# Performance work log

Hardware: AMD Instinct MI355X
Metric: run time of the kernel (lower is better)

The kernel has to match this reference:

```python
import jax, jax.numpy as jnp
import numpy as np


def _normalize(x, axis=-1, eps=1e-12):
    n = jnp.linalg.norm(x, axis=axis, keepdims=True)
    return x / jnp.maximum(n, eps)


def _mlp(x, w1, b1, w2, b2):
    return jnp.maximum(x @ w1 + b1, 0.0) @ w2 + b2


def _quat_mul(a, b):
    # openfold (w, x, y, z) convention, Hamilton product
    aw, ax, ay, az = a[..., 0], a[..., 1], a[..., 2], a[..., 3]
    bw, bx, by, bz = b[..., 0], b[..., 1], b[..., 2], b[..., 3]
    return jnp.stack([
        aw * bw - ax * bx - ay * by - az * bz,
        aw * bx + ax * bw + ay * bz - az * by,
        aw * by - ax * bz + ay * bw + az * bx,
        aw * bz + ax * by - ay * bx + az * bw], axis=-1)


def _quat_rotate(q, v):
    # rotate vector v by unit quaternion q
    w = q[..., :1]
    u = q[..., 1:]
    t = 2.0 * jnp.cross(u, v)
    return v + w * t + jnp.cross(u, t)


def _conj(q):
    return q * jnp.asarray([1.0, -1.0, -1.0, -1.0], dtype=q.dtype)


def setup_inputs() -> dict:
    B, N, P, H, E, M = 2, 384, 128, 64, 32, 64
    key = jax.random.key(0)
    ks = iter(jax.random.split(key, 64))

    def nrm(shape):
        return jax.random.normal(next(ks), shape, dtype=jnp.float32)

    inp = {
        "frames_q": _normalize(nrm((B, N, 4))),
        "frames_x": nrm((B, N, 3)),
        "torsions": nrm((B, N, 7, 2)),
        "h": nrm((B, N, H)),
        "e": nrm((B, N, N, E)),
        "node_mask": jnp.ones((B, N), dtype=bool),
        "pocket_h": nrm((B, P, H)),
        "pocket_e": nrm((B, N, P, E)),
        "pocket_q": _normalize(nrm((B, P, 4))),
        "pocket_x": nrm((B, P, 3)),
        "pocket_mask": jnp.ones((B, P), dtype=bool),
    }
    # 2-layer MLPs with transition_size = 64
    for name, (fin, fout) in {"msg": (2 * H + E + 9, M), "feat": (H + M, H),
                              "tr": (M, 3), "qu": (M, 4), "to": (M, 14)}.items():
        inp[f"{name}_w1"] = nrm((fin, 64)) / np.sqrt(fin)
        inp[f"{name}_b1"] = nrm((64,)) * 0.01
        inp[f"{name}_w2"] = nrm((64, fout)) / np.sqrt(64)
        inp[f"{name}_b2"] = nrm((fout,)) * 0.01
    return inp


def reference(frames_q, frames_x, torsions, h, e, node_mask, pocket_h, pocket_e,
              pocket_q, pocket_x, pocket_mask,
              msg_w1, msg_b1, msg_w2, msg_b2,
              feat_w1, feat_b1, feat_w2, feat_b2,
              tr_w1, tr_b1, tr_w2, tr_b2,
              qu_w1, qu_b1, qu_w2, qu_b2,
              to_w1, to_b1, to_w2, to_b2):
    B, N, Hd = h.shape
    P = pocket_h.shape[-2]

    q_all = jnp.concatenate([frames_q, pocket_q], axis=-2)  # [B, N+P, 4]
    x_all = jnp.concatenate([frames_x, pocket_x], axis=-2)  # [B, N+P, 3]

    eye = jnp.eye(N, dtype=bool)
    mm = jnp.concatenate([
        node_mask[:, :, None] & node_mask[:, None, :] & ~eye,
        node_mask[:, :, None] & pocket_mask[:, None, :]], axis=-1)  # [B, N, N+P]

    vec = frames_x[:, :, None, :] - x_all[:, None, :, :]  # [B, N, N+P, 3]
    d2 = jnp.sum(vec * vec, axis=-1)                       # [B, N, N+P]
    qdot = jnp.abs(jnp.sum(frames_q[:, :, None, :] * q_all[:, None, :, :], axis=-1))

    # global -> local frame of node j applied to node i: R_j^T (x_i - t_j)
    qc = _conj(q_all)[:, None, :, :]                       # [B, 1, N+P, 4]
    local_x = _quat_rotate(qc, vec)                        # [B, N, N+P, 3]
    local_q = _quat_mul(qc, jnp.broadcast_to(frames_q[:, :, None, :], (B, N, N + P, 4)))

    feat = jnp.concatenate([
        jnp.broadcast_to(h[:, :, None, :], (B, N, N + P, Hd)),
        jnp.broadcast_to(jnp.concatenate([h, pocket_h], axis=-2)[:, None, :, :], (B, N, N + P, Hd)),
        jnp.concatenate([e, pocket_e], axis=-2),
        local_x, local_q, d2[..., None], qdot[..., None]], axis=-1)

    m = _mlp(feat, msg_w1, msg_b1, msg_w2, msg_b2) * mm[..., None]  # [B, N, N+P, M]
    msum = jnp.sum(m, axis=-2)                                      # [B, N, M]

    o = _mlp(jnp.concatenate([h, msum], axis=-1), feat_w1, feat_b1, feat_w2, feat_b2)

    dx = _mlp(m, tr_w1, tr_b1, tr_w2, tr_b2) * mm[..., None]        # [B, N, N+P, 3]

    ident = jnp.asarray([1.0, 0.0, 0.0, 0.0], dtype=frames_q.dtype)
    dq = _mlp(msum, qu_w1, qu_b1, qu_w2, qu_b2)
    dq = _normalize(jnp.where(node_mask[..., None], dq, ident))
    upd_q = _quat_mul(frames_q, dq)
    upd_q = _normalize(jnp.where(node_mask[..., None], upd_q, ident))

    qn_all = _normalize(q_all)
    gdx = jnp.sum(_quat_rotate(qn_all[:, None, :, :], dx), axis=-2)  # [B, N, 3]
    n_nb = (node_mask.sum(-1) + pocket_mask.sum(-1) - 1).astype(frames_x.dtype)
    upd_x = frames_x + gdx / n_nb[:, None, None]

    upd_torsions = _normalize(_mlp(msum, to_w1, to_b1, to_w2, to_b2).reshape(torsions.shape))

    return upd_q, upd_x, upd_torsions, o
```

## Files before the change

kernel.cpp:

```cpp
#include <hip/hip_runtime.h>
#include <math.h>

#define BB 2
#define NN 384
#define PP 128
#define HH 64
#define EE 32
#define NP 512
#define K1S 136
#define K2S 72

#define X_OFF (BB*NN*4)
#define T_OFF (X_OFF + BB*NN*3)
#define O_OFF (T_OFF + BB*NN*14)

using bf16x8 = __attribute__((ext_vector_type(8))) __bf16;
using f32x4  = __attribute__((ext_vector_type(4))) float;

__device__ __forceinline__ f32x4 MFMA(bf16x8 a, bf16x8 b, f32x4 c) {
  return __builtin_amdgcn_mfma_f32_16x16x32_bf16(a, b, c, 0, 0, 0);
}
__device__ __forceinline__ bf16x8 LDF(const __bf16* base, int off) {
  return *(const bf16x8*)(base + off);
}
__device__ __forceinline__ bf16x8 pack8(f32x4 lo, f32x4 hi) {
  bf16x8 r;
  r[0]=(__bf16)lo[0]; r[1]=(__bf16)lo[1]; r[2]=(__bf16)lo[2]; r[3]=(__bf16)lo[3];
  r[4]=(__bf16)hi[0]; r[5]=(__bf16)hi[1]; r[6]=(__bf16)hi[2]; r[7]=(__bf16)hi[3];
  return r;
}
__device__ __forceinline__ bf16x8 pack8v(float4 lo, float4 hi) {
  bf16x8 r;
  r[0]=(__bf16)lo.x; r[1]=(__bf16)lo.y; r[2]=(__bf16)lo.z; r[3]=(__bf16)lo.w;
  r[4]=(__bf16)hi.x; r[5]=(__bf16)hi.y; r[6]=(__bf16)hi.z; r[7]=(__bf16)hi.w;
  return r;
}
__device__ __forceinline__ int rowpos(int n) {
  const int t = (n>>5)*2 + ((n>>2)&1);
  const int q = ((n>>3)&3)*4 + (n&3);
  return t*16 + q;
}

__global__ __launch_bounds__(512, 2) void egnn_edge_swapped(
    const float* __restrict__ frames_q, const float* __restrict__ frames_x,
    const float* __restrict__ h, const float* __restrict__ e,
    const int* __restrict__ node_mask,
    const float* __restrict__ pocket_h, const float* __restrict__ pe,
    const float* __restrict__ pocket_q, const float* __restrict__ pocket_x,
    const int* __restrict__ pocket_mask,
    const float* __restrict__ w1, const float* __restrict__ b1,
    const float* __restrict__ w2, const float* __restrict__ b2,
    const float* __restrict__ tw1, const float* __restrict__ tb1,
    const float* __restrict__ tw2, const float* __restrict__ tb2,
    float* __restrict__ msum_ws, float* __restrict__ gdx_ws)
{
  __shared__ __align__(16) __bf16 s_w1p[64*K1S];
  __shared__ __align__(16) __bf16 s_w2p[64*K2S];
  __shared__ __align__(16) __bf16 s_tw1p[64*K2S];
  __shared__ __align__(16) __bf16 s_tw2p[16*K2S];
  __shared__ __align__(16) __bf16 s_geo[NP*16 + 8];
  __shared__ __align__(16) float s_qn[NP*4];
  __shared__ float s_maskf[NP];
  __shared__ __align__(16) float s_b2[64], s_tb1[64];
  __shared__ float s_tb2[4];
  __shared__ float s_msum[64], s_gdx[3];

  const int tid = threadIdx.x;
  const int b = blockIdx.x / NN, i = blockIdx.x % NN;

  for (int idx = tid; idx < 64*128; idx += 512) {
    const int n = idx & 63, k = idx >> 6;
    float v = 0.f;
    if      (k < 64)  v = w1[(64 + k)*64 + n];
    else if (k < 96)  v = w1[(128 + (k-64))*64 + n];
    else if (k < 105) v = w1[(160 + (k-96))*64 + n];
    if (k != 105) s_w1p[rowpos(n)*K1S + k] = (__bf16)v;
  }
  for (int idx = tid; idx < 64*64; idx += 512) {
    const int n = idx & 63, k = idx >> 6;
    s_w2p[rowpos(n)*K2S + k]  = (__bf16)w2[k*64 + n];
    s_tw1p[rowpos(n)*K2S + k] = (__bf16)tw1[k*64 + n];
  }
  for (int idx = tid; idx < 16*64; idx += 512) {
    const int row = idx >> 6, k = idx & 63;
    s_tw2p[row*K2S + k] = (__bf16)((row < 3) ? tw2[k*3 + row] : 0.f);
  }
  if (tid < 64) { s_b2[tid] = b2[tid]; s_tb1[tid] = tb1[tid]; s_msum[tid] = 0.f; }
  if (tid < 8)  s_geo[NP*16 + tid] = (__bf16)0.f;
  if (tid < 3)  { s_tb2[tid] = tb2[tid]; s_gdx[tid] = 0.f; }

  {
    const int n = tid >> 3, part = tid & 7;
    const float* hi = &h[(b*NN + i)*HH];
    float a = 0.f;
#pragma unroll
    for (int c = 0; c < 8; ++c) a = fmaf(hi[part*8 + c], w1[(part*8 + c)*64 + n], a);
    a += __shfl_xor(a, 1); a += __shfl_xor(a, 2); a += __shfl_xor(a, 4);
    if (part == 0) s_w1p[rowpos(n)*K1S + 105] = (__bf16)(a + b1[n]);
  }

  {
    const int j = tid;
    const int maski = node_mask[b*NN + i];
    const float qi0 = frames_q[(b*NN+i)*4+0], qi1 = frames_q[(b*NN+i)*4+1],
                qi2 = frames_q[(b*NN+i)*4+2], qi3 = frames_q[(b*NN+i)*4+3];
    const float xi0 = frames_x[(b*NN+i)*3+0], xi1 = frames_x[(b*NN+i)*3+1],
                xi2 = frames_x[(b*NN+i)*3+2];
    float qj0,qj1,qj2,qj3, xj0,xj1,xj2; int mj;
    if (j < NN) {
      const float4 q4 = *(const float4*)&frames_q[(b*NN+j)*4];
      qj0=q4.x; qj1=q4.y; qj2=q4.z; qj3=q4.w;
      xj0=frames_x[(b*NN+j)*3+0]; xj1=frames_x[(b*NN+j)*3+1]; xj2=frames_x[(b*NN+j)*3+2];
      mj = (node_mask[b*NN+j] != 0) && (j != i);
    } else {
      const int jp = j - NN;
      const float4 q4 = *(const float4*)&pocket_q[(b*PP+jp)*4];
      qj0=q4.x; qj1=q4.y; qj2=q4.z; qj3=q4.w;
      xj0=pocket_x[(b*PP+jp)*3+0]; xj1=pocket_x[(b*PP+jp)*3+1]; xj2=pocket_x[(b*PP+jp)*3+2];
      mj = (pocket_mask[b*PP+jp] != 0);
    }
    const float v0 = xi0 - xj0, v1 = xi1 - xj1, v2 = xi2 - xj2;
    const float d2 = v0*v0 + v1*v1 + v2*v2;
    const float qdot = fabsf(qi0*qj0 + qi1*qj1 + qi2*qj2 + qi3*qj3);
    const float cw = qj0, cx = -qj1, cy = -qj2, cz = -qj3;
    const float t0 = 2.f*(cy*v2 - cz*v1);
    const float t1 = 2.f*(cz*v0 - cx*v2);
    const float t2 = 2.f*(cx*v1 - cy*v0);
    const float lx0 = v0 + cw*t0 + (cy*t2 - cz*t1);
    const float lx1 = v1 + cw*t1 + (cz*t0 - cx*t2);
    const float lx2 = v2 + cw*t2 + (cx*t1 - cy*t0);
    const float lq0 = cw*qi0 - cx*qi1 - cy*qi2 - cz*qi3;
    const float lq1 = cw*qi1 + cx*qi0 + cy*qi3 - cz*qi2;
    const float lq2 = cw*qi2 - cx*qi3 + cy*qi0 + cz*qi1;
    const float lq3 = cw*qi3 + cx*qi2 - cy*qi1 + cz*qi0;
    __bf16* g = &s_geo[j*16];
    g[0]=(__bf16)lx0; g[1]=(__bf16)lx1; g[2]=(__bf16)lx2; g[3]=(__bf16)lq0;
    g[4]=(__bf16)lq1; g[5]=(__bf16)lq2; g[6]=(__bf16)lq3; g[7]=(__bf16)d2;
    g[8]=(__bf16)qdot; g[9]=(__bf16)1.f;
    g[10]=(__bf16)0.f; g[11]=(__bf16)0.f; g[12]=(__bf16)0.f;
    g[13]=(__bf16)0.f; g[14]=(__bf16)0.f; g[15]=(__bf16)0.f;
    s_maskf[j] = (maski && mj) ? 1.f : 0.f;
    const float inv = 1.f / fmaxf(sqrtf(qj0*qj0 + qj1*qj1 + qj2*qj2 + qj3*qj3), 1e-12f);
    float4* qn = (float4*)&s_qn[j*4];
    *qn = make_float4(qj0*inv, qj1*inv, qj2*inv, qj3*inv);
  }
  __syncthreads();

  const int wv = tid >> 6, lane = tid & 63;
  const int l15 = lane & 15, lg = lane >> 4;

  bf16x8 tw2f[2];
  tw2f[0] = *(const bf16x8*)&s_tw2p[l15*K2S +  0 + lg*8];
  tw2f[1] = *(const bf16x8*)&s_tw2p[l15*K2S + 32 + lg*8];
  const float tb2r0 = s_tb2[0], tb2r1 = s_tb2[1], tb2r2 = s_tb2[2];

  float msacc[16];
#pragma unroll
  for (int v = 0; v < 16; ++v) msacc[v] = 0.f;
  float gx0 = 0.f, gx1 = 0.f, gx2 = 0.f;

  const int o1base = l15*K1S + lg*8;
  const int o2base = l15*K2S + lg*8;
  const int obbase = lg*8;

#define LOADSTRIP(JB0, H0_,H1_,H2_,H3_,E0_,E1_) do {                        \
    const int jb_ = (JB0);                                                  \
    const int j_ = jb_ + l15;                                               \
    const float *hj_, *ej_;                                                 \
    if (jb_ < NN) {                                                         \
      hj_ = &h[(b*NN + j_)*HH];                                             \
      ej_ = &e[((b*NN + i)*NN + j_)*EE];                                    \
    } else {                                                                \
      const int jp_ = j_ - NN;                                              \
      hj_ = &pocket_h[(b*PP + jp_)*HH];                                     \
      ej_ = &pe[((b*NN + i)*PP + jp_)*EE];                                  \
    }                                                                       \
    H0_ = *(const float4*)&hj_[lg*8];                                       \
    H1_ = *(const float4*)&hj_[lg*8 + 4];                                   \
    H2_ = *(const float4*)&hj_[32 + lg*8];                                  \
    H3_ = *(const float4*)&hj_[32 + lg*8 + 4];                              \
    E0_ = *(const float4*)&ej_[lg*8];                                       \
    E1_ = *(const float4*)&ej_[lg*8 + 4];                                   \
  } while (0)

#pragma unroll
  for (int ss = 0; ss < 2; ++ss) {
    int o1 = o1base; asm volatile("" : "+v"(o1));
    int o2 = o2base; asm volatile("" : "+v"(o2));
    int ob = obbase; asm volatile("" : "+v"(ob));

    const int jbA = wv*64 + ss*32;
    const int jbB = jbA + 16;
    const int jA = jbA + l15, jB = jbB + l15;

    float4 hA0,hA1,hA2,hA3,eA0,eA1, hB0,hB1,hB2,hB3,eB0,eB1;
    LOADSTRIP(jbA, hA0,hA1,hA2,hA3,eA0,eA1);
    LOADSTRIP(jbB, hB0,hB1,hB2,hB3,eB0,eB1);
    const float maskA = s_maskf[jA];
    const float maskB = s_maskf[jB];

    const bf16x8 bfA0 = pack8v(hA0, hA1);
    const bf16x8 bfA1 = pack8v(hA2, hA3);
    const bf16x8 bfA2 = pack8v(eA0, eA1);
    const bf16x8 bfA3 = *(const bf16x8*)&s_geo[(lg < 2) ? (jA*16 + lg*8) : NP*16];
    const bf16x8 bfB0 = pack8v(hB0, hB1);
    const bf16x8 bfB1 = pack8v(hB2, hB3);
    const bf16x8 bfB2 = pack8v(eB0, eB1);
    const bf16x8 bfB3 = *(const bf16x8*)&s_geo[(lg < 2) ? (jB*16 + lg*8) : NP*16];

    const f32x4 zero4 = {0.f, 0.f, 0.f, 0.f};

    bf16x8 hbA0, hbA1, hbB0, hbB1;
    {
      f32x4 aA0, aA1, aB0, aB1;
      {
        const bf16x8 F0 = LDF(s_w1p, o1 + 0*16*K1S +  0);
        const bf16x8 F1 = LDF(s_w1p, o1 + 0*16*K1S + 32);
        const bf16x8 F2 = LDF(s_w1p, o1 + 0*16*K1S + 64);
        const bf16x8 F3 = LDF(s_w1p, o1 + 0*16*K1S + 96);
        aA0 = MFMA(F0,bfA0,zero4); aA0 = MFMA(F1,bfA1,aA0); aA0 = MFMA(F2,bfA2,aA0); aA0 = MFMA(F3,bfA3,aA0);
        aB0 = MFMA(F0,bfB0,zero4); aB0 = MFMA(F1,bfB1,aB0); aB0 = MFMA(F2,bfB2,aB0); aB0 = MFMA(F3,bfB3,aB0);
      }
      {
        const bf16x8 F0 = LDF(s_w1p, o1 + 1*16*K1S +  0);
        const bf16x8 F1 = LDF(s_w1p, o1 + 1*16*K1S + 32);
        const bf16x8 F2 = LDF(s_w1p, o1 + 1*16*K1S + 64);
        const bf16x8 F3 = LDF(s_w1p, o1 + 1*16*K1S + 96);
        aA1 = MFMA(F0,bfA0,zero4); aA1 = MFMA(F1,bfA1,aA1); aA1 = MFMA(F2,bfA2,aA1); aA1 = MFMA(F3,bfA3,aA1);
        aB1 = MFMA(F0,bfB0,zero4); aB1 = MFMA(F1,bfB1,aB1); aB1 = MFMA(F2,bfB2,aB1); aB1 = MFMA(F3,bfB3,aB1);
      }
#pragma unroll
      for (int r = 0; r < 4; ++r) {
        aA0[r] = fmaxf(aA0[r], 0.f); aA1[r] = fmaxf(aA1[r], 0.f);
        aB0[r] = fmaxf(aB0[r], 0.f); aB1[r] = fmaxf(aB1[r], 0.f);
      }
      hbA0 = pack8(aA0, aA1); hbB0 = pack8(aB0, aB1);
      {
        const bf16x8 F0 = LDF(s_w1p, o1 + 2*16*K1S +  0);
        const bf16x8 F1 = LDF(s_w1p, o1 + 2*16*K1S + 32);
        const bf16x8 F2 = LDF(s_w1p, o1 + 2*16*K1S + 64);
        const bf16x8 F3 = LDF(s_w1p, o1 + 2*16*K1S + 96);
        aA0 = MFMA(F0,bfA0,zero4); aA0 = MFMA(F1,bfA1,aA0); aA0 = MFMA(F2,bfA2,aA0); aA0 = MFMA(F3,bfA3,aA0);
        aB0 = MFMA(F0,bfB0,zero4); aB0 = MFMA(F1,bfB1,aB0); aB0 = MFMA(F2,bfB2,aB0); aB0 = MFMA(F3,bfB3,aB0);
      }
      {
        const bf16x8 F0 = LDF(s_w1p, o1 + 3*16*K1S +  0);
        const bf16x8 F1 = LDF(s_w1p, o1 + 3*16*K1S + 32);
        const bf16x8 F2 = LDF(s_w1p, o1 + 3*16*K1S + 64);
        const bf16x8 F3 = LDF(s_w1p, o1 + 3*16*K1S + 96);
        aA1 = MFMA(F0,bfA0,zero4); aA1 = MFMA(F1,bfA1,aA1); aA1 = MFMA(F2,bfA2,aA1); aA1 = MFMA(F3,bfA3,aA1);
        aB1 = MFMA(F0,bfB0,zero4); aB1 = MFMA(F1,bfB1,aB1); aB1 = MFMA(F2,bfB2,aB1); aB1 = MFMA(F3,bfB3,aB1);
      }
#pragma unroll
      for (int r = 0; r < 4; ++r) {
        aA0[r] = fmaxf(aA0[r], 0.f); aA1[r] = fmaxf(aA1[r], 0.f);
        aB0[r] = fmaxf(aB0[r], 0.f); aB1[r] = fmaxf(aB1[r], 0.f);
      }
      hbA1 = pack8(aA0, aA1); hbB1 = pack8(aB0, aB1);
    }

    bf16x8 mbA0, mbA1, mbB0, mbB1;
    {
      f32x4 cA0, cA1, cB0, cB1;
      {
        const bf16x8 F0 = LDF(s_w2p, o2 + 0*16*K2S +  0);
        const bf16x8 F1 = LDF(s_w2p, o2 + 0*16*K2S + 32);
        cA0 = MFMA(F0,hbA0,zero4); cA0 = MFMA(F1,hbA1,cA0);
        cB0 = MFMA(F0,hbB0,zero4); cB0 = MFMA(F1,hbB1,cB0);
      }
      {
        const bf16x8 F0 = LDF(s_w2p, o2 + 1*16*K2S +  0);
        const bf16x8 F1 = LDF(s_w2p, o2 + 1*16*K2S + 32);
        cA1 = MFMA(F0,hbA0,zero4); cA1 = MFMA(F1,hbA1,cA1);
        cB1 = MFMA(F0,hbB0,zero4); cB1 = MFMA(F1,hbB1,cB1);
      }
      const f32x4 bb0 = *(const f32x4*)&s_b2[ob + 0];
      const f32x4 bb1 = *(const f32x4*)&s_b2[ob + 4];
#pragma unroll
      for (int r = 0; r < 4; ++r) {
        cA0[r] = (cA0[r] + bb0[r]) * maskA;  cB0[r] = (cB0[r] + bb0[r]) * maskB;
        cA1[r] = (cA1[r] + bb1[r]) * maskA;  cB1[r] = (cB1[r] + bb1[r]) * maskB;
        msacc[0*4+r] += cA0[r] + cB0[r];
        msacc[1*4+r] += cA1[r] + cB1[r];
      }
      mbA0 = pack8(cA0, cA1); mbB0 = pack8(cB0, cB1);
      {
        const bf16x8 F0 = LDF(s_w2p, o2 + 2*16*K2S +  0);
        const bf16x8 F1 = LDF(s_w2p, o2 + 2*16*K2S + 32);
        cA0 = MFMA(F0,hbA0,zero4); cA0 = MFMA(F1,hbA1,cA0);
        cB0 = MFMA(F0,hbB0,zero4); cB0 = MFMA(F1,hbB1,cB0);
      }
      {
        const bf16x8 F0 = LDF(s_w2p, o2 + 3*16*K2S +  0);
        const bf16x8 F1 = LDF(s_w2p, o2 + 3*16*K2S + 32);
        cA1 = MFMA(F0,hbA0,zero4); cA1 = MFMA(F1,hbA1,cA1);
        cB1 = MFMA(F0,hbB0,zero4); cB1 = MFMA(F1,hbB1,cB1);
      }
      const f32x4 bb2 = *(const f32x4*)&s_b2[ob + 32];
      const f32x4 bb3 = *(const f32x4*)&s_b2[ob + 36];
#pragma unroll
      for (int r = 0; r < 4; ++r) {
        cA0[r] = (cA0[r] + bb2[r]) * maskA;  cB0[r] = (cB0[r] + bb2[r]) * maskB;
        cA1[r] = (cA1[r] + bb3[r]) * maskA;  cB1[r] = (cB1[r] + bb3[r]) * maskB;
        msacc[2*4+r] += cA0[r] + cB0[r];
        msacc[3*4+r] += cA1[r] + cB1[r];
      }
      mbA1 = pack8(cA0, cA1); mbB1 = pack8(cB0, cB1);
    }

    bf16x8 thbA0, thbA1, thbB0, thbB1;
    {
      f32x4 dA0, dA1, dB0, dB1;
      {
        const bf16x8 F0 = LDF(s_tw1p, o2 + 0*16*K2S +  0);
        const bf16x8 F1 = LDF(s_tw1p, o2 + 0*16*K2S + 32);
        dA0 = MFMA(F0,mbA0,zero4); dA0 = MFMA(F1,mbA1,dA0);
        dB0 = MFMA(F0,mbB0,zero4); dB0 = MFMA(F1,mbB1,dB0);
      }
      {
        const bf16x8 F0 = LDF(s_tw1p, o2 + 1*16*K2S +  0);
        const bf16x8 F1 = LDF(s_tw1p, o2 + 1*16*K2S + 32);
        dA1 = MFMA(F0,mbA0,zero4); dA1 = MFMA(F1,mbA1,dA1);
        dB1 = MFMA(F0,mbB0,zero4); dB1 = MFMA(F1,mbB1,dB1);
      }
      {
        const f32x4 tb0 = *(const f32x4*)&s_tb1[ob + 0];
        const f32x4 tb1v = *(const f32x4*)&s_tb1[ob + 4];
#pragma unroll
        for (int r = 0; r < 4; ++r) {
          dA0[r] = fmaxf(dA0[r] + tb0[r], 0.f);  dB0[r] = fmaxf(dB0[r] + tb0[r], 0.f);
          dA1[r] = fmaxf(dA1[r] + tb1v[r], 0.f); dB1[r] = fmaxf(dB1[r] + tb1v[r], 0.f);
        }
      }
      thbA0 = pack8(dA0, dA1); thbB0 = pack8(dB0, dB1);
      {
        const bf16x8 F0 = LDF(s_tw1p, o2 + 2*16*K2S +  0);
        const bf16x8 F1 = LDF(s_tw1p, o2 + 2*16*K2S + 32);
        dA0 = MFMA(F0,mbA0,zero4); dA0 = MFMA(F1,mbA1,dA0);
        dB0 = MFMA(F0,mbB0,zero4); dB0 = MFMA(F1,mbB1,dB0);
      }
      {
        const bf16x8 F0 = LDF(s_tw1p, o2 + 3*16*K2S +  0);
        const bf16x8 F1 = LDF(s_tw1p, o2 + 3*16*K2S + 32);
        dA1 = MFMA(F0,mbA0,zero4); dA1 = MFMA(F1,mbA1,dA1);
        dB1 = MFMA(F0,mbB0,zero4); dB1 = MFMA(F1,mbB1,dB1);
      }
      {
        const f32x4 tb2v = *(const f32x4*)&s_tb1[ob + 32];
        const f32x4 tb3v = *(const f32x4*)&s_tb1[ob + 36];
#pragma unroll
        for (int r = 0; r < 4; ++r) {
          dA0[r] = fmaxf(dA0[r] + tb2v[r], 0.f);  dB0[r] = fmaxf(dB0[r] + tb2v[r], 0.f);
          dA1[r] = fmaxf(dA1[r] + tb3v[r], 0.f);  dB1[r] = fmaxf(dB1[r] + tb3v[r], 0.f);
        }
      }
      thbA1 = pack8(dA0, dA1); thbB1 = pack8(dB0, dB1);
    }

    f32x4 daccA = MFMA(tw2f[0], thbA0, zero4);
    daccA = MFMA(tw2f[1], thbA1, daccA);
    f32x4 daccB = MFMA(tw2f[0], thbB0, zero4);
    daccB = MFMA(tw2f[1], thbB1, daccB);

    if (lg == 0) {
      {
        const float dx0 = (daccA[0] + tb2r0) * maskA;
        const float dx1 = (daccA[1] + tb2r1) * maskA;
        const float dx2 = (daccA[2] + tb2r2) * maskA;
        const float4 qn = *(const float4*)&s_qn[jA*4];
        const float w = qn.x, ux = qn.y, uy = qn.z, uz = qn.w;
        const float r0 = 2.f*(uy*dx2 - uz*dx1);
        const float r1 = 2.f*(uz*dx0 - ux*dx2);
        const float r2 = 2.f*(ux*dx1 - uy*dx0);
        gx0 += dx0 + w*r0 + (uy*r2 - uz*r1);
        gx1 += dx1 + w*r1 + (uz*r0 - ux*r2);
        gx2 += dx2 + w*r2 + (ux*r1 - uy*r0);
      }
      {
        const float dx0 = (daccB[0] + tb2r0) * maskB;
        const float dx1 = (daccB[1] + tb2r1) * maskB;
        const float dx2 = (daccB[2] + tb2r2) * maskB;
        const float4 qn = *(const float4*)&s_qn[jB*4];
        const float w = qn.x, ux = qn.y, uy = qn.z, uz = qn.w;
        const float r0 = 2.f*(uy*dx2 - uz*dx1);
        const float r1 = 2.f*(uz*dx0 - ux*dx2);
        const float r2 = 2.f*(ux*dx1 - uy*dx0);
        gx0 += dx0 + w*r0 + (uy*r2 - uz*r1);
        gx1 += dx1 + w*r1 + (uz*r0 - ux*r2);
        gx2 += dx2 + w*r2 + (ux*r1 - uy*r0);
      }
    }
  }
#undef LOADSTRIP

#pragma unroll
  for (int v = 0; v < 16; ++v) {
    float x = msacc[v];
    x += __shfl_xor(x, 1); x += __shfl_xor(x, 2);
    x += __shfl_xor(x, 4); x += __shfl_xor(x, 8);
    if (l15 == 0) {
      const int n2 = (v>>3)*32 + lg*8 + ((v>>2)&1)*4 + (v&3);
      atomicAdd(&s_msum[n2], x);
    }
  }
  {
    float v0 = (lg == 0) ? gx0 : 0.f;
    float v1 = (lg == 0) ? gx1 : 0.f;
    float v2 = (lg == 0) ? gx2 : 0.f;
#pragma unroll
    for (int sft = 1; sft < 64; sft <<= 1) {
      v0 += __shfl_xor(v0, sft); v1 += __shfl_xor(v1, sft); v2 += __shfl_xor(v2, sft);
    }
    if (lane == 0) { atomicAdd(&s_gdx[0], v0); atomicAdd(&s_gdx[1], v1); atomicAdd(&s_gdx[2], v2); }
  }
  __syncthreads();
  if (tid < 64) msum_ws[(b*NN + i)*64 + tid] = s_msum[tid];
  if (tid >= 64 && tid < 67) gdx_ws[(b*NN + i)*3 + (tid - 64)] = s_gdx[tid - 64];
}

__global__ __launch_bounds__(64) void egnn_node_kernel(
    const float* __restrict__ frames_q, const float* __restrict__ frames_x,
    const float* __restrict__ h,
    const int* __restrict__ node_mask, const int* __restrict__ pocket_mask,
    const float* __restrict__ fw1, const float* __restrict__ fb1,
    const float* __restrict__ fw2, const float* __restrict__ fb2,
    const float* __restrict__ qw1, const float* __restrict__ qb1,
    const float* __restrict__ qw2, const float* __restrict__ qb2,
    const float* __restrict__ tow1, const float* __restrict__ tob1,
    const float* __restrict__ tow2, const float* __restrict__ tob2,
    const float* __restrict__ msum_ws, const float* __restrict__ gdx_ws,
    float* __restrict__ out)
{
  const int t  = threadIdx.x;
  const int bi = blockIdx.x;
  const int b = bi / NN, i = bi % NN;
  __shared__ float s_h[64], s_ms[64], s_hid[64], s_tmp[16];

  s_h[t]  = h[(b*NN+i)*HH + t];
  s_ms[t] = msum_ws[(b*NN+i)*64 + t];

  int cnt = 0;
  for (int k = t; k < NN; k += 64) cnt += (node_mask[b*NN+k] != 0);
  for (int k = t; k < PP; k += 64) cnt += (pocket_mask[b*PP+k] != 0);
  cnt += __shfl_xor(cnt,1); cnt += __shfl_xor(cnt,2); cnt += __shfl_xor(cnt,4);
  cnt += __shfl_xor(cnt,8); cnt += __shfl_xor(cnt,16); cnt += __shfl_xor(cnt,32);
  const float n_nb = (float)(cnt - 1);

  __syncthreads();
  float a = fb1[t];
  for (int k = 0; k < 64; ++k) a = fmaf(s_h[k],  fw1[k*64 + t], a);
  for (int k = 0; k < 64; ++k) a = fmaf(s_ms[k], fw1[(64+k)*64 + t], a);
  s_hid[t] = fmaxf(a, 0.f);
  __syncthreads();
  float ov = fb2[t];
  for (int k = 0; k < 64; ++k) ov = fmaf(s_hid[k], fw2[k*64 + t], ov);
  out[O_OFF + (b*NN+i)*64 + t] = ov;

  __syncthreads();
  float aq = qb1[t];
  for (int k = 0; k < 64; ++k) aq = fmaf(s_ms[k], qw1[k*64 + t], aq);
  s_hid[t] = fmaxf(aq, 0.f);
  __syncthreads();
  if (t < 4) {
    float d = qb2[t];
    for (int k = 0; k < 64; ++k) d = fmaf(s_hid[k], qw2[k*4 + t], d);
    s_tmp[t] = d;
  }
  __syncthreads();
  if (t == 0) {
    const int mi = node_mask[b*NN+i];
    float d0,d1,d2,d3;
    if (mi) { d0=s_tmp[0]; d1=s_tmp[1]; d2=s_tmp[2]; d3=s_tmp[3]; }
    else    { d0=1.f; d1=0.f; d2=0.f; d3=0.f; }
    float nrm = fmaxf(sqrtf(d0*d0+d1*d1+d2*d2+d3*d3), 1e-12f);
    d0/=nrm; d1/=nrm; d2/=nrm; d3/=nrm;
    const float q0=frames_q[(b*NN+i)*4+0], q1=frames_q[(b*NN+i)*4+1],
                q2=frames_q[(b*NN+i)*4+2], q3=frames_q[(b*NN+i)*4+3];
    float u0 = q0*d0 - q1*d1 - q2*d2 - q3*d3;
    float u1 = q0*d1 + q1*d0 + q2*d3 - q3*d2;
    float u2 = q0*d2 - q1*d3 + q2*d0 + q3*d1;
    float u3 = q0*d3 + q1*d2 - q2*d1 + q3*d0;
    if (!mi) { u0=1.f; u1=0.f; u2=0.f; u3=0.f; }
    float nrm2 = fmaxf(sqrtf(u0*u0+u1*u1+u2*u2+u3*u3), 1e-12f);
    out[(b*NN+i)*4+0]=u0/nrm2; out[(b*NN+i)*4+1]=u1/nrm2;
    out[(b*NN+i)*4+2]=u2/nrm2; out[(b*NN+i)*4+3]=u3/nrm2;
  }
  if (t < 3) {
    out[X_OFF + (b*NN+i)*3 + t] = frames_x[(b*NN+i)*3+t] + gdx_ws[(b*NN+i)*3+t] / n_nb;
  }

  __syncthreads();
  float at = tob1[t];
  for (int k = 0; k < 64; ++k) at = fmaf(s_ms[k], tow1[k*64 + t], at);
  s_hid[t] = fmaxf(at, 0.f);
  __syncthreads();
  if (t < 14) {
    float v = tob2[t];
    for (int k = 0; k < 64; ++k) v = fmaf(s_hid[k], tow2[k*14 + t], v);
    s_tmp[t] = v;
  }
  __syncthreads();
  if (t < 14) {
    const int p = t & ~1;
    const float a0 = s_tmp[p], a1 = s_tmp[p+1];
    const float nrm = fmaxf(sqrtf(a0*a0 + a1*a1), 1e-12f);
    out[T_OFF + (b*NN+i)*14 + t] = s_tmp[t] / nrm;
  }
}

extern "C" void kernel_launch(void* const* d_in, const int* in_sizes, int n_in,
                              void* d_out, int out_size, void* d_ws, size_t ws_size,
                              hipStream_t stream) {
  const float* frames_q    = (const float*)d_in[0];
  const float* frames_x    = (const float*)d_in[1];
  const float* h           = (const float*)d_in[3];
  const float* e           = (const float*)d_in[4];
  const int*   node_mask   = (const int*)d_in[5];
  const float* pocket_h    = (const float*)d_in[6];
  const float* pocket_e    = (const float*)d_in[7];
  const float* pocket_q    = (const float*)d_in[8];
  const float* pocket_x    = (const float*)d_in[9];
  const int*   pocket_mask = (const int*)d_in[10];
  const float* msg_w1 = (const float*)d_in[11];
  const float* msg_b1 = (const float*)d_in[12];
  const float* msg_w2 = (const float*)d_in[13];
  const float* msg_b2 = (const float*)d_in[14];
  const float* feat_w1 = (const float*)d_in[15];
  const float* feat_b1 = (const float*)d_in[16];
  const float* feat_w2 = (const float*)d_in[17];
  const float* feat_b2 = (const float*)d_in[18];
  const float* tr_w1 = (const float*)d_in[19];
  const float* tr_b1 = (const float*)d_in[20];
  const float* tr_w2 = (const float*)d_in[21];
  const float* tr_b2 = (const float*)d_in[22];
  const float* qu_w1 = (const float*)d_in[23];
  const float* qu_b1 = (const float*)d_in[24];
  const float* qu_w2 = (const float*)d_in[25];
  const float* qu_b2 = (const float*)d_in[26];
  const float* to_w1 = (const float*)d_in[27];
  const float* to_b1 = (const float*)d_in[28];
  const float* to_w2 = (const float*)d_in[29];
  const float* to_b2 = (const float*)d_in[30];

  float* out = (float*)d_out;
  float* msum_ws = (float*)d_ws;
  float* gdx_ws  = msum_ws + BB*NN*64;

  egnn_edge_swapped<<<dim3(BB*NN), dim3(512), 0, stream>>>(
      frames_q, frames_x, h, e, node_mask,
      pocket_h, pocket_e, pocket_q, pocket_x, pocket_mask,
      msg_w1, msg_b1, msg_w2, msg_b2,
      tr_w1, tr_b1, tr_w2, tr_b2,
      msum_ws, gdx_ws);

  egnn_node_kernel<<<dim3(BB*NN), dim3(64), 0, stream>>>(
      frames_q, frames_x, h, node_mask, pocket_mask,
      feat_w1, feat_b1, feat_w2, feat_b2,
      qu_w1, qu_b1, qu_w2, qu_b2,
      to_w1, to_b1, to_w2, to_b2,
      msum_ws, gdx_ws, out);
}
```

Measured before the change: 65.02 us.

## Make edge kernel persistent with 1024-thread blocks looping over three nodes

The edge kernel becomes persistent: 256 blocks of 1024 threads each process three query nodes in turn. Packed weights are loaded into shared memory once per block instead of once per node. Each wave now handles one 32-neighbour strip per node rather than two. This cuts redundant weight staging and launch overhead. In exchange it adds barriers between nodes, caps residency at one block per CU, and removes overlap across nodes within a CU.

```diff
diff --git a/kernel.cpp b/kernel.cpp
--- a/kernel.cpp
+++ b/kernel.cpp
@@ -41,7 +41,7 @@
   return t*16 + q;
 }
 
-__global__ __launch_bounds__(512, 2) void egnn_edge_swapped(
+__global__ __launch_bounds__(1024, 1) void egnn_edge_persist(
     const float* __restrict__ frames_q, const float* __restrict__ frames_x,
     const float* __restrict__ h, const float* __restrict__ e,
     const int* __restrict__ node_mask,
@@ -66,9 +66,8 @@
   __shared__ float s_msum[64], s_gdx[3];
 
   const int tid = threadIdx.x;
-  const int b = blockIdx.x / NN, i = blockIdx.x % NN;
-
-  for (int idx = tid; idx < 64*128; idx += 512) {
+
+  for (int idx = tid; idx < 64*128; idx += 1024) {
     const int n = idx & 63, k = idx >> 6;
     float v = 0.f;
     if      (k < 64)  v = w1[(64 + k)*64 + n];
@@ -76,74 +75,18 @@
     else if (k < 105) v = w1[(160 + (k-96))*64 + n];
     if (k != 105) s_w1p[rowpos(n)*K1S + k] = (__bf16)v;
   }
-  for (int idx = tid; idx < 64*64; idx += 512) {
+  for (int idx = tid; idx < 64*64; idx += 1024) {
     const int n = idx & 63, k = idx >> 6;
     s_w2p[rowpos(n)*K2S + k]  = (__bf16)w2[k*64 + n];
     s_tw1p[rowpos(n)*K2S + k] = (__bf16)tw1[k*64 + n];
   }
-  for (int idx = tid; idx < 16*64; idx += 512) {
+  for (int idx = tid; idx < 16*64; idx += 1024) {
     const int row = idx >> 6, k = idx & 63;
     s_tw2p[row*K2S + k] = (__bf16)((row < 3) ? tw2[k*3 + row] : 0.f);
   }
-  if (tid < 64) { s_b2[tid] = b2[tid]; s_tb1[tid] = tb1[tid]; s_msum[tid] = 0.f; }
+  if (tid < 64) { s_b2[tid] = b2[tid]; s_tb1[tid] = tb1[tid]; }
   if (tid < 8)  s_geo[NP*16 + tid] = (__bf16)0.f;
-  if (tid < 3)  { s_tb2[tid] = tb2[tid]; s_gdx[tid] = 0.f; }
-
-  {
-    const int n = tid >> 3, part = tid & 7;
-    const float* hi = &h[(b*NN + i)*HH];
-    float a = 0.f;
-#pragma unroll
-    for (int c = 0; c < 8; ++c) a = fmaf(hi[part*8 + c], w1[(part*8 + c)*64 + n], a);
-    a += __shfl_xor(a, 1); a += __shfl_xor(a, 2); a += __shfl_xor(a, 4);
-    if (part == 0) s_w1p[rowpos(n)*K1S + 105] = (__bf16)(a + b1[n]);
-  }
-
-  {
-    const int j = tid;
-    const int maski = node_mask[b*NN + i];
-    const float qi0 = frames_q[(b*NN+i)*4+0], qi1 = frames_q[(b*NN+i)*4+1],
-                qi2 = frames_q[(b*NN+i)*4+2], qi3 = frames_q[(b*NN+i)*4+3];
-    const float xi0 = frames_x[(b*NN+i)*3+0], xi1 = frames_x[(b*NN+i)*3+1],
-                xi2 = frames_x[(b*NN+i)*3+2];
-    float qj0,qj1,qj2,qj3, xj0,xj1,xj2; int mj;
-    if (j < NN) {
-      const float4 q4 = *(const float4*)&frames_q[(b*NN+j)*4];
-      qj0=q4.x; qj1=q4.y; qj2=q4.z; qj3=q4.w;
-      xj0=frames_x[(b*NN+j)*3+0]; xj1=frames_x[(b*NN+j)*3+1]; xj2=frames_x[(b*NN+j)*3+2];
-      mj = (node_mask[b*NN+j] != 0) && (j != i);
-    } else {
-      const int jp = j - NN;
-      const float4 q4 = *(const float4*)&pocket_q[(b*PP+jp)*4];
-      qj0=q4.x; qj1=q4.y; qj2=q4.z; qj3=q4.w;
-      xj0=pocket_x[(b*PP+jp)*3+0]; xj1=pocket_x[(b*PP+jp)*3+1]; xj2=pocket_x[(b*PP+jp)*3+2];
-      mj = (pocket_mask[b*PP+jp] != 0);
-    }
-    const float v0 = xi0 - xj0, v1 = xi1 - xj1, v2 = xi2 - xj2;
-    const float d2 = v0*v0 + v1*v1 + v2*v2;
-    const float qdot = fabsf(qi0*qj0 + qi1*qj1 + qi2*qj2 + qi3*qj3);
-    const float cw = qj0, cx = -qj1, cy = -qj2, cz = -qj3;
-    const float t0 = 2.f*(cy*v2 - cz*v1);
-    const float t1 = 2.f*(cz*v0 - cx*v2);
-    const float t2 = 2.f*(cx*v1 - cy*v0);
-    const float lx0 = v0 + cw*t0 + (cy*t2 - cz*t1);
-    const float lx1 = v1 + cw*t1 + (cz*t0 - cx*t2);
-    const float lx2 = v2 + cw*t2 + (cx*t1 - cy*t0);
-    const float lq0 = cw*qi0 - cx*qi1 - cy*qi2 - cz*qi3;
-    const float lq1 = cw*qi1 + cx*qi0 + cy*qi3 - cz*qi2;
-    const float lq2 = cw*qi2 - cx*qi3 + cy*qi0 + cz*qi1;
-    const float lq3 = cw*qi3 + cx*qi2 - cy*qi1 + cz*qi0;
-    __bf16* g = &s_geo[j*16];
-    g[0]=(__bf16)lx0; g[1]=(__bf16)lx1; g[2]=(__bf16)lx2; g[3]=(__bf16)lq0;
-    g[4]=(__bf16)lq1; g[5]=(__bf16)lq2; g[6]=(__bf16)lq3; g[7]=(__bf16)d2;
-    g[8]=(__bf16)qdot; g[9]=(__bf16)1.f;
-    g[10]=(__bf16)0.f; g[11]=(__bf16)0.f; g[12]=(__bf16)0.f;
-    g[13]=(__bf16)0.f; g[14]=(__bf16)0.f; g[15]=(__bf16)0.f;
-    s_maskf[j] = (maski && mj) ? 1.f : 0.f;
-    const float inv = 1.f / fmaxf(sqrtf(qj0*qj0 + qj1*qj1 + qj2*qj2 + qj3*qj3), 1e-12f);
-    float4* qn = (float4*)&s_qn[j*4];
-    *qn = make_float4(qj0*inv, qj1*inv, qj2*inv, qj3*inv);
-  }
+  if (tid < 3)  s_tb2[tid] = tb2[tid];
   __syncthreads();
 
   const int wv = tid >> 6, lane = tid & 63;
@@ -153,11 +96,6 @@
   tw2f[0] = *(const bf16x8*)&s_tw2p[l15*K2S +  0 + lg*8];
   tw2f[1] = *(const bf16x8*)&s_tw2p[l15*K2S + 32 + lg*8];
   const float tb2r0 = s_tb2[0], tb2r1 = s_tb2[1], tb2r2 = s_tb2[2];
-
-  float msacc[16];
-#pragma unroll
-  for (int v = 0; v < 16; ++v) msacc[v] = 0.f;
-  float gx0 = 0.f, gx1 = 0.f, gx2 = 0.f;
 
   const int o1base = l15*K1S + lg*8;
   const int o2base = l15*K2S + lg*8;
@@ -183,239 +121,311 @@
     E1_ = *(const float4*)&ej_[lg*8 + 4];                                   \
   } while (0)
 
-#pragma unroll
-  for (int ss = 0; ss < 2; ++ss) {
-    int o1 = o1base; asm volatile("" : "+v"(o1));
-    int o2 = o2base; asm volatile("" : "+v"(o2));
-    int ob = obbase; asm volatile("" : "+v"(ob));
-
-    const int jbA = wv*64 + ss*32;
-    const int jbB = jbA + 16;
-    const int jA = jbA + l15, jB = jbB + l15;
-
-    float4 hA0,hA1,hA2,hA3,eA0,eA1, hB0,hB1,hB2,hB3,eB0,eB1;
-    LOADSTRIP(jbA, hA0,hA1,hA2,hA3,eA0,eA1);
-    LOADSTRIP(jbB, hB0,hB1,hB2,hB3,eB0,eB1);
-    const float maskA = s_maskf[jA];
-    const float maskB = s_maskf[jB];
-
-    const bf16x8 bfA0 = pack8v(hA0, hA1);
-    const bf16x8 bfA1 = pack8v(hA2, hA3);
-    const bf16x8 bfA2 = pack8v(eA0, eA1);
-    const bf16x8 bfA3 = *(const bf16x8*)&s_geo[(lg < 2) ? (jA*16 + lg*8) : NP*16];
-    const bf16x8 bfB0 = pack8v(hB0, hB1);
-    const bf16x8 bfB1 = pack8v(hB2, hB3);
-    const bf16x8 bfB2 = pack8v(eB0, eB1);
-    const bf16x8 bfB3 = *(const bf16x8*)&s_geo[(lg < 2) ? (jB*16 + lg*8) : NP*16];
-
-    const f32x4 zero4 = {0.f, 0.f, 0.f, 0.f};
-
-    bf16x8 hbA0, hbA1, hbB0, hbB1;
+#pragma unroll 1
+  for (int rep = 0; rep < 3; ++rep) {
+    const int ni = (int)blockIdx.x + rep*256;
+    const int b = ni / NN, i = ni % NN;
+
+    __syncthreads();
+    if (tid < 64) s_msum[tid] = 0.f;
+    if (tid < 3)  s_gdx[tid] = 0.f;
+
     {
-      f32x4 aA0, aA1, aB0, aB1;
+      const int n = tid >> 4, part = tid & 15;
+      const float* hi = &h[(b*NN + i)*HH];
+      float a = 0.f;
+#pragma unroll
+      for (int c = 0; c < 4; ++c) a = fmaf(hi[part*4 + c], w1[(part*4 + c)*64 + n], a);
+      a += __shfl_xor(a, 1); a += __shfl_xor(a, 2);
+      a += __shfl_xor(a, 4); a += __shfl_xor(a, 8);
+      if (part == 0) s_w1p[rowpos(n)*K1S + 105] = (__bf16)(a + b1[n]);
+    }
+
+    if (tid < NP) {
+      const int j = tid;
+      const int maski = node_mask[b*NN + i];
+      const float qi0 = frames_q[(b*NN+i)*4+0], qi1 = frames_q[(b*NN+i)*4+1],
+                  qi2 = frames_q[(b*NN+i)*4+2], qi3 = frames_q[(b*NN+i)*4+3];
+      const float xi0 = frames_x[(b*NN+i)*3+0], xi1 = frames_x[(b*NN+i)*3+1],
+                  xi2 = frames_x[(b*NN+i)*3+2];
+      float qj0,qj1,qj2,qj3, xj0,xj1,xj2; int mj;
+      if (j < NN) {
+        const float4 q4 = *(const float4*)&frames_q[(b*NN+j)*4];
+        qj0=q4.x; qj1=q4.y; qj2=q4.z; qj3=q4.w;
+        xj0=frames_x[(b*NN+j)*3+0]; xj1=frames_x[(b*NN+j)*3+1]; xj2=frames_x[(b*NN+j)*3+2];
+        mj = (node_mask[b*NN+j] != 0) && (j != i);
+      } else {
+        const int jp = j - NN;
+        const float4 q4 = *(const float4*)&pocket_q[(b*PP+jp)*4];
+        qj0=q4.x; qj1=q4.y; qj2=q4.z; qj3=q4.w;
+        xj0=pocket_x[(b*PP+jp)*3+0]; xj1=pocket_x[(b*PP+jp)*3+1]; xj2=pocket_x[(b*PP+jp)*3+2];
+        mj = (pocket_mask[b*PP+jp] != 0);
+      }
+      const float v0 = xi0 - xj0, v1 = xi1 - xj1, v2 = xi2 - xj2;
+      const float d2 = v0*v0 + v1*v1 + v2*v2;
+      const float qdot = fabsf(qi0*qj0 + qi1*qj1 + qi2*qj2 + qi3*qj3);
+      const float cw = qj0, cx = -qj1, cy = -qj2, cz = -qj3;
+      const float t0 = 2.f*(cy*v2 - cz*v1);
+      const float t1 = 2.f*(cz*v0 - cx*v2);
+      const float t2 = 2.f*(cx*v1 - cy*v0);
+      const float lx0 = v0 + cw*t0 + (cy*t2 - cz*t1);
+      const float lx1 = v1 + cw*t1 + (cz*t0 - cx*t2);
+      const float lx2 = v2 + cw*t2 + (cx*t1 - cy*t0);
+      const float lq0 = cw*qi0 - cx*qi1 - cy*qi2 - cz*qi3;
+      const float lq1 = cw*qi1 + cx*qi0 + cy*qi3 - cz*qi2;
+      const float lq2 = cw*qi2 - cx*qi3 + cy*qi0 + cz*qi1;
+      const float lq3 = cw*qi3 + cx*qi2 - cy*qi1 + cz*qi0;
+      __bf16* g = &s_geo[j*16];
+      g[0]=(__bf16)lx0; g[1]=(__bf16)lx1; g[2]=(__bf16)lx2; g[3]=(__bf16)lq0;
+      g[4]=(__bf16)lq1; g[5]=(__bf16)lq2; g[6]=(__bf16)lq3; g[7]=(__bf16)d2;
+      g[8]=(__bf16)qdot; g[9]=(__bf16)1.f;
+      g[10]=(__bf16)0.f; g[11]=(__bf16)0.f; g[12]=(__bf16)0.f;
+      g[13]=(__bf16)0.f; g[14]=(__bf16)0.f; g[15]=(__bf16)0.f;
+      s_maskf[j] = (maski && mj) ? 1.f : 0.f;
+      const float inv = 1.f / fmaxf(sqrtf(qj0*qj0 + qj1*qj1 + qj2*qj2 + qj3*qj3), 1e-12f);
+      float4* qn = (float4*)&s_qn[j*4];
+      *qn = make_float4(qj0*inv, qj1*inv, qj2*inv, qj3*inv);
+    }
+    __syncthreads();
+
+    float msacc[16];
+#pragma unroll
+    for (int v = 0; v < 16; ++v) msacc[v] = 0.f;
+    float gx0 = 0.f, gx1 = 0.f, gx2 = 0.f;
+
+    {
+      int o1 = o1base; asm volatile("" : "+v"(o1));
+      int o2 = o2base; asm volatile("" : "+v"(o2));
+      int ob = obbase; asm volatile("" : "+v"(ob));
+
+      const int jbA = wv*32;
+      const int jbB = jbA + 16;
+      const int jA = jbA + l15, jB = jbB + l15;
+
+      float4 hA0,hA1,hA2,hA3,eA0,eA1, hB0,hB1,hB2,hB3,eB0,eB1;
+      LOADSTRIP(jbA, hA0,hA1,hA2,hA3,eA0,eA1);
+      LOADSTRIP(jbB, hB0,hB1,hB2,hB3,eB0,eB1);
+      const float maskA = s_maskf[jA];
+      const float maskB = s_maskf[jB];
+
+      const bf16x8 bfA0 = pack8v(hA0, hA1);
+      const bf16x8 bfA1 = pack8v(hA2, hA3);
+      const bf16x8 bfA2 = pack8v(eA0, eA1);
+      const bf16x8 bfA3 = *(const bf16x8*)&s_geo[(lg < 2) ? (jA*16 + lg*8) : NP*16];
+      const bf16x8 bfB0 = pack8v(hB0, hB1);
+      const bf16x8 bfB1 = pack8v(hB2, hB3);
+      const bf16x8 bfB2 = pack8v(eB0, eB1);
+      const bf16x8 bfB3 = *(const bf16x8*)&s_geo[(lg < 2) ? (jB*16 + lg*8) : NP*16];
+
+      const f32x4 zero4 = {0.f, 0.f, 0.f, 0.f};
+
+      bf16x8 hbA0, hbA1, hbB0, hbB1;
       {
-        const bf16x8 F0 = LDF(s_w1p, o1 + 0*16*K1S +  0);
-        const bf16x8 F1 = LDF(s_w1p, o1 + 0*16*K1S + 32);
-        const bf16x8 F2 = LDF(s_w1p, o1 + 0*16*K1S + 64);
-        const bf16x8 F3 = LDF(s_w1p, o1 + 0*16*K1S + 96);
-        aA0 = MFMA(F0,bfA0,zero4); aA0 = MFMA(F1,bfA1,aA0); aA0 = MFMA(F2,bfA2,aA0); aA0 = MFMA(F3,bfA3,aA0);
-        aB0 = MFMA(F0,bfB0,zero4); aB0 = MFMA(F1,bfB1,aB0); aB0 = MFMA(F2,bfB2,aB0); aB0 = MFMA(F3,bfB3,aB0);
-      }
+        f32x4 aA0, aA1, aB0, aB1;
+        {
+          const bf16x8 F0 = LDF(s_w1p, o1 + 0*16*K1S +  0);
+          const bf16x8 F1 = LDF(s_w1p, o1 + 0*16*K1S + 32);
+          const bf16x8 F2 = LDF(s_w1p, o1 + 0*16*K1S + 64);
+          const bf16x8 F3 = LDF(s_w1p, o1 + 0*16*K1S + 96);
+          aA0 = MFMA(F0,bfA0,zero4); aA0 = MFMA(F1,bfA1,aA0); aA0 = MFMA(F2,bfA2,aA0); aA0 = MFMA(F3,bfA3,aA0);
+          aB0 = MFMA(F0,bfB0,zero4); aB0 = MFMA(F1,bfB1,aB0); aB0 = MFMA(F2,bfB2,aB0); aB0 = MFMA(F3,bfB3,aB0);
+        }
+        {
+          const bf16x8 F0 = LDF(s_w1p, o1 + 1*16*K1S +  0);
+          const bf16x8 F1 = LDF(s_w1p, o1 + 1*16*K1S + 32);
+          const bf16x8 F2 = LDF(s_w1p, o1 + 1*16*K1S + 64);
+          const bf16x8 F3 = LDF(s_w1p, o1 + 1*16*K1S + 96);
+          aA1 = MFMA(F0,bfA0,zero4); aA1 = MFMA(F1,bfA1,aA1); aA1 = MFMA(F2,bfA2,aA1); aA1 = MFMA(F3,bfA3,aA1);
+          aB1 = MFMA(F0,bfB0,zero4); aB1 = MFMA(F1,bfB1,aB1); aB1 = MFMA(F2,bfB2,aB1); aB1 = MFMA(F3,bfB3,aB1);
+        }
+#pragma unroll
+        for (int r = 0; r < 4; ++r) {
+          aA0[r] = fmaxf(aA0[r], 0.f); aA1[r] = fmaxf(aA1[r], 0.f);
+          aB0[r] = fmaxf(aB0[r], 0.f); aB1[r] = fmaxf(aB1[r], 0.f);
+        }
+        hbA0 = pack8(aA0, aA1); hbB0 = pack8(aB0, aB1);
+        {
+          const bf16x8 F0 = LDF(s_w1p, o1 + 2*16*K1S +  0);
+          const bf16x8 F1 = LDF(s_w1p, o1 + 2*16*K1S + 32);
+          const bf16x8 F2 = LDF(s_w1p, o1 + 2*16*K1S + 64);
+          const bf16x8 F3 = LDF(s_w1p, o1 + 2*16*K1S + 96);
+          aA0 = MFMA(F0,bfA0,zero4); aA0 = MFMA(F1,bfA1,aA0); aA0 = MFMA(F2,bfA2,aA0); aA0 = MFMA(F3,bfA3,aA0);
+          aB0 = MFMA(F0,bfB0,zero4); aB0 = MFMA(F1,bfB1,aB0); aB0 = MFMA(F2,bfB2,aB0); aB0 = MFMA(F3,bfB3,aB0);
+        }
+        {
+          const bf16x8 F0 = LDF(s_w1p, o1 + 3*16*K1S +  0);
+          const bf16x8 F1 = LDF(s_w1p, o1 + 3*16*K1S + 32);
+          const bf16x8 F2 = LDF(s_w1p, o1 + 3*16*K1S + 64);
+          const bf16x8 F3 = LDF(s_w1p, o1 + 3*16*K1S + 96);
+          aA1 = MFMA(F0,bfA0,zero4); aA1 = MFMA(F1,bfA1,aA1); aA1 = MFMA(F2,bfA2,aA1); aA1 = MFMA(F3,bfA3,aA1);
+          aB1 = MFMA(F0,bfB0,zero4); aB1 = MFMA(F1,bfB1,aB1); aB1 = MFMA(F2,bfB2,aB1); aB1 = MFMA(F3,bfB3,aB1);
+        }
+#pragma unroll
+        for (int r = 0; r < 4; ++r) {
+          aA0[r] = fmaxf(aA0[r], 0.f); aA1[r] = fmaxf(aA1[r], 0.f);
+          aB0[r] = fmaxf(aB0[r], 0.f); aB1[r] = fmaxf(aB1[r], 0.f);
+        }
+        hbA1 = pack8(aA0, aA1); hbB1 = pack8(aB0, aB1);
+      }
+
+      bf16x8 mbA0, mbA1, mbB0, mbB1;
       {
-        const bf16x8 F0 = LDF(s_w1p, o1 + 1*16*K1S +  0);
-        const bf16x8 F1 = LDF(s_w1p, o1 + 1*16*K1S + 32);
-        const bf16x8 F2 = LDF(s_w1p, o1 + 1*16*K1S + 64);
-        const bf16x8 F3 = LDF(s_w1p, o1 + 1*16*K1S + 96);
-        aA1 = MFMA(F0,bfA0,zero4); aA1 = MFMA(F1,bfA1,aA1); aA1 = MFMA(F2,bfA2,aA1); aA1 = MFMA(F3,bfA3,aA1);
-        aB1 = MFMA(F0,bfB0,zero4); aB1 = MFMA(F1,bfB1,aB1); aB1 = MFMA(F2,bfB2,aB1); aB1 = MFMA(F3,bfB3,aB1);
-      }
-#pragma unroll
-      for (int r = 0; r < 4; ++r) {
-        aA0[r] = fmaxf(aA0[r], 0.f); aA1[r] = fmaxf(aA1[r], 0.f);
-        aB0[r] = fmaxf(aB0[r], 0.f); aB1[r] = fmaxf(aB1[r], 0.f);
-      }
-      hbA0 = pack8(aA0, aA1); hbB0 = pack8(aB0, aB1);
+        f32x4 cA0, cA1, cB0, cB1;
+        {
+          const bf16x8 F0 = LDF(s_w2p, o2 + 0*16*K2S +  0);
+          const bf16x8 F1 = LDF(s_w2p, o2 + 0*16*K2S + 32);
+          cA0 = MFMA(F0,hbA0,zero4); cA0 = MFMA(F1,hbA1,cA0);
+          cB0 = MFMA(F0,hbB0,zero4); cB0 = MFMA(F1,hbB1,cB0);
+        }
+        {
+          const bf16x8 F0 = LDF(s_w2p, o2 + 1*16*K2S +  0);
+          const bf16x8 F1 = LDF(s_w2p, o2 + 1*16*K2S + 32);
+          cA1 = MFMA(F0,hbA0,zero4); cA1 = MFMA(F1,hbA1,cA1);
+          cB1 = MFMA(F0,hbB0,zero4); cB1 = MFMA(F1,hbB1,cB1);
+        }
+        const f32x4 bb0 = *(const f32x4*)&s_b2[ob + 0];
+        const f32x4 bb1 = *(const f32x4*)&s_b2[ob + 4];
+#pragma unroll
+        for (int r = 0; r < 4; ++r) {
+          cA0[r] = (cA0[r] + bb0[r]) * maskA;  cB0[r] = (cB0[r] + bb0[r]) * maskB;
+          cA1[r] = (cA1[r] + bb1[r]) * maskA;  cB1[r] = (cB1[r] + bb1[r]) * maskB;
+          msacc[0*4+r] += cA0[r] + cB0[r];
+          msacc[1*4+r] += cA1[r] + cB1[r];
+        }
+        mbA0 = pack8(cA0, cA1); mbB0 = pack8(cB0, cB1);
+        {
+          const bf16x8 F0 = LDF(s_w2p, o2 + 2*16*K2S +  0);
+          const bf16x8 F1 = LDF(s_w2p, o2 + 2*16*K2S + 32);
+          cA0 = MFMA(F0,hbA0,zero4); cA0 = MFMA(F1,hbA1,cA0);
+          cB0 = MFMA(F0,hbB0,zero4); cB0 = MFMA(F1,hbB1,cB0);
+        }
+        {
+          const bf16x8 F0 = LDF(s_w2p, o2 + 3*16*K2S +  0);
+          const bf16x8 F1 = LDF(s_w2p, o2 + 3*16*K2S + 32);
+          cA1 = MFMA(F0,hbA0,zero4); cA1 = MFMA(F1,hbA1,cA1);
+          cB1 = MFMA(F0,hbB0,zero4); cB1 = MFMA(F1,hbB1,cB1);
+        }
+        const f32x4 bb2 = *(const f32x4*)&s_b2[ob + 32];
+        const f32x4 bb3 = *(const f32x4*)&s_b2[ob + 36];
+#pragma unroll
+        for (int r = 0; r < 4; ++r) {
+          cA0[r] = (cA0[r] + bb2[r]) * maskA;  cB0[r] = (cB0[r] + bb2[r]) * maskB;
+          cA1[r] = (cA1[r] + bb3[r]) * maskA;  cB1[r] = (cB1[r] + bb3[r]) * maskB;
+          msacc[2*4+r] += cA0[r] + cB0[r];
+          msacc[3*4+r] += cA1[r] + cB1[r];
+        }
+        mbA1 = pack8(cA0, cA1); mbB1 = pack8(cB0, cB1);
+      }
+
+      bf16x8 thbA0, thbA1, thbB0, thbB1;
       {
-        const bf16x8 F0 = LDF(s_w1p, o1 + 2*16*K1S +  0);
-        const bf16x8 F1 = LDF(s_w1p, o1 + 2*16*K1S + 32);
-        const bf16x8 F2 = LDF(s_w1p, o1 + 2*16*K1S + 64);
-        const bf16x8 F3 = LDF(s_w1p, o1 + 2*16*K1S + 96);
-        aA0 = MFMA(F0,bfA0,zero4); aA0 = MFMA(F1,bfA1,aA0); aA0 = MFMA(F2,bfA2,aA0); aA0 = MFMA(F3,bfA3,aA0);
-        aB0 = MFMA(F0,bfB0,zero4); aB0 = MFMA(F1,bfB1,aB0); aB0 = MFMA(F2,bfB2,aB0); aB0 = MFMA(F3,bfB3,aB0);
-      }
-      {
-        const bf16x8 F0 = LDF(s_w1p, o1 + 3*16*K1S +  0);
-        const bf16x8 F1 = LDF(s_w1p, o1 + 3*16*K1S + 32);
-        const bf16x8 F2 = LDF(s_w1p, o1 + 3*16*K1S + 64);
-        const bf16x8 F3 = LDF(s_w1p, o1 + 3*16*K1S + 96);
-        aA1 = MFMA(F0,bfA0,zero4); aA1 = MFMA(F1,bfA1,aA1); aA1 = MFMA(F2,bfA2,aA1); aA1 = MFMA(F3,bfA3,aA1);
-        aB1 = MFMA(F0,bfB0,zero4); aB1 = MFMA(F1,bfB1,aB1); aB1 = MFMA(F2,bfB2,aB1); aB1 = MFMA(F3,bfB3,aB1);
-      }
-#pragma unroll
-      for (int r = 0; r < 4; ++r) {
-        aA0[r] = fmaxf(aA0[r], 0.f); aA1[r] = fmaxf(aA1[r], 0.f);
-        aB0[r] = fmaxf(aB0[r], 0.f); aB1[r] = fmaxf(aB1[r], 0.f);
-      }
-      hbA1 = pack8(aA0, aA1); hbB1 = pack8(aB0, aB1);
+        f32x4 dA0, dA1, dB0, dB1;
+        {
+          const bf16x8 F0 = LDF(s_tw1p, o2 + 0*16*K2S +  0);
+          const bf16x8 F1 = LDF(s_tw1p, o2 + 0*16*K2S + 32);
+          dA0 = MFMA(F0,mbA0,zero4); dA0 = MFMA(F1,mbA1,dA0);
+          dB0 = MFMA(F0,mbB0,zero4); dB0 = MFMA(F1,mbB1,dB0);
+        }
+        {
+          const bf16x8 F0 = LDF(s_tw1p, o2 + 1*16*K2S +  0);
+          const bf16x8 F1 = LDF(s_tw1p, o2 + 1*16*K2S + 32);
+          dA1 = MFMA(F0,mbA0,zero4); dA1 = MFMA(F1,mbA1,dA1);
+          dB1 = MFMA(F0,mbB0,zero4); dB1 = MFMA(F1,mbB1,dB1);
+        }
+        {
+          const f32x4 tb0 = *(const f32x4*)&s_tb1[ob + 0];
+          const f32x4 tb1v = *(const f32x4*)&s_tb1[ob + 4];
+#pragma unroll
+          for (int r = 0; r < 4; ++r) {
+            dA0[r] = fmaxf(dA0[r] + tb0[r], 0.f);  dB0[r] = fmaxf(dB0[r] + tb0[r], 0.f);
+            dA1[r] = fmaxf(dA1[r] + tb1v[r], 0.f); dB1[r] = fmaxf(dB1[r] + tb1v[r], 0.f);
+          }
+        }
+        thbA0 = pack8(dA0, dA1); thbB0 = pack8(dB0, dB1);
+        {
+          const bf16x8 F0 = LDF(s_tw1p, o2 + 2*16*K2S +  0);
+          const bf16x8 F1 = LDF(s_tw1p, o2 + 2*16*K2S + 32);
+          dA0 = MFMA(F0,mbA0,zero4); dA0 = MFMA(F1,mbA1,dA0);
+          dB0 = MFMA(F0,mbB0,zero4); dB0 = MFMA(F1,mbB1,dB0);
+        }
+        {
+          const bf16x8 F0 = LDF(s_tw1p, o2 + 3*16*K2S +  0);
+          const bf16x8 F1 = LDF(s_tw1p, o2 + 3*16*K2S + 32);
+          dA1 = MFMA(F0,mbA0,zero4); dA1 = MFMA(F1,mbA1,dA1);
+          dB1 = MFMA(F0,mbB0,zero4); dB1 = MFMA(F1,mbB1,dB1);
+        }
+        {
+          const f32x4 tb2v = *(const f32x4*)&s_tb1[ob + 32];
+          const f32x4 tb3v = *(const f32x4*)&s_tb1[ob + 36];
+#pragma unroll
+          for (int r = 0; r < 4; ++r) {
+            dA0[r] = fmaxf(dA0[r] + tb2v[r], 0.f);  dB0[r] = fmaxf(dB0[r] + tb2v[r], 0.f);
+            dA1[r] = fmaxf(dA1[r] + tb3v[r], 0.f);  dB1[r] = fmaxf(dB1[r] + tb3v[r], 0.f);
+          }
+        }
+        thbA1 = pack8(dA0, dA1); thbB1 = pack8(dB0, dB1);
+      }
+
+      f32x4 daccA = MFMA(tw2f[0], thbA0, zero4);
+      daccA = MFMA(tw2f[1], thbA1, daccA);
+      f32x4 daccB = MFMA(tw2f[0], thbB0, zero4);
+      daccB = MFMA(tw2f[1], thbB1, daccB);
+
+      if (lg == 0) {
+        {
+          const float dx0 = (daccA[0] + tb2r0) * maskA;
+          const float dx1 = (daccA[1] + tb2r1) * maskA;
+          const float dx2 = (daccA[2] + tb2r2) * maskA;
+          const float4 qn = *(const float4*)&s_qn[jA*4];
+          const float w = qn.x, ux = qn.y, uy = qn.z, uz = qn.w;
+          const float r0 = 2.f*(uy*dx2 - uz*dx1);
+          const float r1 = 2.f*(uz*dx0 - ux*dx2);
+          const float r2 = 2.f*(ux*dx1 - uy*dx0);
+          gx0 += dx0 + w*r0 + (uy*r2 - uz*r1);
+          gx1 += dx1 + w*r1 + (uz*r0 - ux*r2);
+          gx2 += dx2 + w*r2 + (ux*r1 - uy*r0);
+        }
+        {
+          const float dx0 = (daccB[0] + tb2r0) * maskB;
+          const float dx1 = (daccB[1] + tb2r1) * maskB;
+          const float dx2 = (daccB[2] + tb2r2) * maskB;
+          const float4 qn = *(const float4*)&s_qn[jB*4];
+          const float w = qn.x, ux = qn.y, uy = qn.z, uz = qn.w;
+          const float r0 = 2.f*(uy*dx2 - uz*dx1);
+          const float r1 = 2.f*(uz*dx0 - ux*dx2);
+          const float r2 = 2.f*(ux*dx1 - uy*dx0);
+          gx0 += dx0 + w*r0 + (uy*r2 - uz*r1);
+          gx1 += dx1 + w*r1 + (uz*r0 - ux*r2);
+          gx2 += dx2 + w*r2 + (ux*r1 - uy*r0);
+        }
+      }
     }
 
-    bf16x8 mbA0, mbA1, mbB0, mbB1;
+#pragma unroll
+    for (int v = 0; v < 16; ++v) {
+      float x = msacc[v];
+      x += __shfl_xor(x, 1); x += __shfl_xor(x, 2);
+      x += __shfl_xor(x, 4); x += __shfl_xor(x, 8);
+      if (l15 == 0) {
+        const int n2 = (v>>3)*32 + lg*8 + ((v>>2)&1)*4 + (v&3);
+        atomicAdd(&s_msum[n2], x);
+      }
+    }
     {
-      f32x4 cA0, cA1, cB0, cB1;
-      {
-        const bf16x8 F0 = LDF(s_w2p, o2 + 0*16*K2S +  0);
-        const bf16x8 F1 = LDF(s_w2p, o2 + 0*16*K2S + 32);
-        cA0 = MFMA(F0,hbA0,zero4); cA0 = MFMA(F1,hbA1,cA0);
-        cB0 = MFMA(F0,hbB0,zero4); cB0 = MFMA(F1,hbB1,cB0);
-      }
-      {
-        const bf16x8 F0 = LDF(s_w2p, o2 + 1*16*K2S +  0);
-        const bf16x8 F1 = LDF(s_w2p, o2 + 1*16*K2S + 32);
-        cA1 = MFMA(F0,hbA0,zero4); cA1 = MFMA(F1,hbA1,cA1);
-        cB1 = MFMA(F0,hbB0,zero4); cB1 = MFMA(F1,hbB1,cB1);
-      }
-      const f32x4 bb0 = *(const f32x4*)&s_b2[ob + 0];
-      const f32x4 bb1 = *(const f32x4*)&s_b2[ob + 4];
-#pragma unroll
-      for (int r = 0; r < 4; ++r) {
-        cA0[r] = (cA0[r] + bb0[r]) * maskA;  cB0[r] = (cB0[r] + bb0[r]) * maskB;
-        cA1[r] = (cA1[r] + bb1[r]) * maskA;  cB1[r] = (cB1[r] + bb1[r]) * maskB;
-        msacc[0*4+r] += cA0[r] + cB0[r];
-        msacc[1*4+r] += cA1[r] + cB1[r];
-      }
-      mbA0 = pack8(cA0, cA1); mbB0 = pack8(cB0, cB1);
-      {
-        const bf16x8 F0 = LDF(s_w2p, o2 + 2*16*K2S +  0);
-        const bf16x8 F1 = LDF(s_w2p, o2 + 2*16*K2S + 32);
-        cA0 = MFMA(F0,hbA0,zero4); cA0 = MFMA(F1,hbA1,cA0);
-        cB0 = MFMA(F0,hbB0,zero4); cB0 = MFMA(F1,hbB1,cB0);
-      }
-      {
-        const bf16x8 F0 = LDF(s_w2p, o2 + 3*16*K2S +  0);
-        const bf16x8 F1 = LDF(s_w2p, o2 + 3*16*K2S + 32);
-        cA1 = MFMA(F0,hbA0,zero4); cA1 = MFMA(F1,hbA1,cA1);
-        cB1 = MFMA(F0,hbB0,zero4); cB1 = MFMA(F1,hbB1,cB1);
-      }
-      const f32x4 bb2 = *(const f32x4*)&s_b2[ob + 32];
-      const f32x4 bb3 = *(const f32x4*)&s_b2[ob + 36];
-#pragma unroll
-      for (int r = 0; r < 4; ++r) {
-        cA0[r] = (cA0[r] + bb2[r]) * maskA;  cB0[r] = (cB0[r] + bb2[r]) * maskB;
-        cA1[r] = (cA1[r] + bb3[r]) * maskA;  cB1[r] = (cB1[r] + bb3[r]) * maskB;
-        msacc[2*4+r] += cA0[r] + cB0[r];
-        msacc[3*4+r] += cA1[r] + cB1[r];
-      }
-      mbA1 = pack8(cA0, cA1); mbB1 = pack8(cB0, cB1);
+      float v0 = (lg == 0) ? gx0 : 0.f;
+      float v1 = (lg == 0) ? gx1 : 0.f;
+      float v2 = (lg == 0) ? gx2 : 0.f;
+#pragma unroll
+      for (int sft = 1; sft < 64; sft <<= 1) {
+        v0 += __shfl_xor(v0, sft); v1 += __shfl_xor(v1, sft); v2 += __shfl_xor(v2, sft);
+      }
+      if (lane == 0) { atomicAdd(&s_gdx[0], v0); atomicAdd(&s_gdx[1], v1); atomicAdd(&s_gdx[2], v2); }
     }
-
-    bf16x8 thbA0, thbA1, thbB0, thbB1;
-    {
-      f32x4 dA0, dA1, dB0, dB1;
-      {
-        const bf16x8 F0 = LDF(s_tw1p, o2 + 0*16*K2S +  0);
-        const bf16x8 F1 = LDF(s_tw1p, o2 + 0*16*K2S + 32);
-        dA0 = MFMA(F0,mbA0,zero4); dA0 = MFMA(F1,mbA1,dA0);
-        dB0 = MFMA(F0,mbB0,zero4); dB0 = MFMA(F1,mbB1,dB0);
-      }
-      {
-        const bf16x8 F0 = LDF(s_tw1p, o2 + 1*16*K2S +  0);
-        const bf16x8 F1 = LDF(s_tw1p, o2 + 1*16*K2S + 32);
-        dA1 = MFMA(F0,mbA0,zero4); dA1 = MFMA(F1,mbA1,dA1);
-        dB1 = MFMA(F0,mbB0,zero4); dB1 = MFMA(F1,mbB1,dB1);
-      }
-      {
-        const f32x4 tb0 = *(const f32x4*)&s_tb1[ob + 0];
-        const f32x4 tb1v = *(const f32x4*)&s_tb1[ob + 4];
-#pragma unroll
-        for (int r = 0; r < 4; ++r) {
-          dA0[r] = fmaxf(dA0[r] + tb0[r], 0.f);  dB0[r] = fmaxf(dB0[r] + tb0[r], 0.f);
-          dA1[r] = fmaxf(dA1[r] + tb1v[r], 0.f); dB1[r] = fmaxf(dB1[r] + tb1v[r], 0.f);
-        }
-      }
-      thbA0 = pack8(dA0, dA1); thbB0 = pack8(dB0, dB1);
-      {
-        const bf16x8 F0 = LDF(s_tw1p, o2 + 2*16*K2S +  0);
-        const bf16x8 F1 = LDF(s_tw1p, o2 + 2*16*K2S + 32);
-        dA0 = MFMA(F0,mbA0,zero4); dA0 = MFMA(F1,mbA1,dA0);
-        dB0 = MFMA(F0,mbB0,zero4); dB0 = MFMA(F1,mbB1,dB0);
-      }
-      {
-        const bf16x8 F0 = LDF(s_tw1p, o2 + 3*16*K2S +  0);
-        const bf16x8 F1 = LDF(s_tw1p, o2 + 3*16*K2S + 32);
-        dA1 = MFMA(F0,mbA0,zero4); dA1 = MFMA(F1,mbA1,dA1);
-        dB1 = MFMA(F0,mbB0,zero4); dB1 = MFMA(F1,mbB1,dB1);
-      }
-      {
-        const f32x4 tb2v = *(const f32x4*)&s_tb1[ob + 32];
-        const f32x4 tb3v = *(const f32x4*)&s_tb1[ob + 36];
-#pragma unroll
-        for (int r = 0; r < 4; ++r) {
-          dA0[r] = fmaxf(dA0[r] + tb2v[r], 0.f);  dB0[r] = fmaxf(dB0[r] + tb2v[r], 0.f);
-          dA1[r] = fmaxf(dA1[r] + tb3v[r], 0.f);  dB1[r] = fmaxf(dB1[r] + tb3v[r], 0.f);
-        }
-      }
-      thbA1 = pack8(dA0, dA1); thbB1 = pack8(dB0, dB1);
-    }
-
-    f32x4 daccA = MFMA(tw2f[0], thbA0, zero4);
-    daccA = MFMA(tw2f[1], thbA1, daccA);
-    f32x4 daccB = MFMA(tw2f[0], thbB0, zero4);
-    daccB = MFMA(tw2f[1], thbB1, daccB);
-
-    if (lg == 0) {
-      {
-        const float dx0 = (daccA[0] + tb2r0) * maskA;
-        const float dx1 = (daccA[1] + tb2r1) * maskA;
-        const float dx2 = (daccA[2] + tb2r2) * maskA;
-        const float4 qn = *(const float4*)&s_qn[jA*4];
-        const float w = qn.x, ux = qn.y, uy = qn.z, uz = qn.w;
-        const float r0 = 2.f*(uy*dx2 - uz*dx1);
-        const float r1 = 2.f*(uz*dx0 - ux*dx2);
-        const float r2 = 2.f*(ux*dx1 - uy*dx0);
-        gx0 += dx0 + w*r0 + (uy*r2 - uz*r1);
-        gx1 += dx1 + w*r1 + (uz*r0 - ux*r2);
-        gx2 += dx2 + w*r2 + (ux*r1 - uy*r0);
-      }
-      {
-        const float dx0 = (daccB[0] + tb2r0) * maskB;
-        const float dx1 = (daccB[1] + tb2r1) * maskB;
-        const float dx2 = (daccB[2] + tb2r2) * maskB;
-        const float4 qn = *(const float4*)&s_qn[jB*4];
-        const float w = qn.x, ux = qn.y, uy = qn.z, uz = qn.w;
-        const float r0 = 2.f*(uy*dx2 - uz*dx1);
-        const float r1 = 2.f*(uz*dx0 - ux*dx2);
-        const float r2 = 2.f*(ux*dx1 - uy*dx0);
-        gx0 += dx0 + w*r0 + (uy*r2 - uz*r1);
-        gx1 += dx1 + w*r1 + (uz*r0 - ux*r2);
-        gx2 += dx2 + w*r2 + (ux*r1 - uy*r0);
-      }
-    }
+    __syncthreads();
+    if (tid < 64) msum_ws[ni*64 + tid] = s_msum[tid];
+    if (tid >= 64 && tid < 67) gdx_ws[ni*3 + (tid - 64)] = s_gdx[tid - 64];
   }
 #undef LOADSTRIP
-
-#pragma unroll
-  for (int v = 0; v < 16; ++v) {
-    float x = msacc[v];
-    x += __shfl_xor(x, 1); x += __shfl_xor(x, 2);
-    x += __shfl_xor(x, 4); x += __shfl_xor(x, 8);
-    if (l15 == 0) {
-      const int n2 = (v>>3)*32 + lg*8 + ((v>>2)&1)*4 + (v&3);
-      atomicAdd(&s_msum[n2], x);
-    }
-  }
-  {
-    float v0 = (lg == 0) ? gx0 : 0.f;
-    float v1 = (lg == 0) ? gx1 : 0.f;
-    float v2 = (lg == 0) ? gx2 : 0.f;
-#pragma unroll
-    for (int sft = 1; sft < 64; sft <<= 1) {
-      v0 += __shfl_xor(v0, sft); v1 += __shfl_xor(v1, sft); v2 += __shfl_xor(v2, sft);
-    }
-    if (lane == 0) { atomicAdd(&s_gdx[0], v0); atomicAdd(&s_gdx[1], v1); atomicAdd(&s_gdx[2], v2); }
-  }
-  __syncthreads();
-  if (tid < 64) msum_ws[(b*NN + i)*64 + tid] = s_msum[tid];
-  if (tid >= 64 && tid < 67) gdx_ws[(b*NN + i)*3 + (tid - 64)] = s_gdx[tid - 64];
 }
 
 __global__ __launch_bounds__(64) void egnn_node_kernel(
@@ -546,7 +556,7 @@
   float* msum_ws = (float*)d_ws;
   float* gdx_ws  = msum_ws + BB*NN*64;
 
-  egnn_edge_swapped<<<dim3(BB*NN), dim3(512), 0, stream>>>(
+  egnn_edge_persist<<<dim3(256), dim3(1024), 0, stream>>>(
       frames_q, frames_x, h, e, node_mask,
       pocket_h, pocket_e, pocket_q, pocket_x, pocket_mask,
       msg_w1, msg_b1, msg_w2, msg_b2,
```

New measurement: 59.48 us. 8.5% less time.
